# Optimization experiments

Hardware: AMD Instinct MI355X
Metric: run time of the kernel (lower is better)

The kernel has to match this reference:

```python
import jax, jax.numpy as jnp
import numpy as np

NUM_HEADS = 16
EMBED_DIM = 1024
LN_EPS = 1e-5


def setup_inputs() -> dict:
    key = jax.random.key(0)
    ks = jax.random.split(key, 9)
    B, S, D = 4, 1024, EMBED_DIM
    return {
        "query": jax.random.normal(ks[0], (B, S, D), dtype=jnp.float32),
        "key": jax.random.normal(ks[1], (B, S, D), dtype=jnp.float32),
        "value": jax.random.normal(ks[2], (B, S, D), dtype=jnp.float32),
        "W_query": 0.01 * jax.random.normal(ks[3], (D, D), dtype=jnp.float32),
        "W_key": 0.01 * jax.random.normal(ks[4], (D, D), dtype=jnp.float32),
        "W_value": 0.01 * jax.random.normal(ks[5], (D, D), dtype=jnp.float32),
        "W_output": 0.01 * jax.random.normal(ks[6], (D, D), dtype=jnp.float32),
        "ln_gamma": jnp.ones((D,), dtype=jnp.float32),
        "ln_beta": jnp.zeros((D,), dtype=jnp.float32),
        "mask": 1,
    }


def _split_heads(x):
    # [B,S,D] -> [H,B,S,d]; torch split(dim=-1)+stack(dim=0) gives head h = cols h*d:(h+1)*d
    B, S, D = x.shape
    d = D // NUM_HEADS
    return jnp.moveaxis(x.reshape(B, S, NUM_HEADS, d), 2, 0)


def reference(query, key, value, W_query, W_key, W_value, W_output, ln_gamma, ln_beta, mask):
    B, S, D = query.shape
    d = D // NUM_HEADS
    q = _split_heads(query @ W_query)   # [H,B,S,d]
    k = _split_heads(key @ W_key)       # [H,B,S,d]
    v = _split_heads(value @ W_value)   # [H,B,S,d]
    scale = jnp.asarray(np.sqrt(d), dtype=q.dtype)
    scores = jnp.einsum("hbqd,hbkd->hbqk", q, k) / scale  # [H,B,S,S]
    attn = jax.nn.softmax(scores, axis=-1)
    if mask:
        # post-hoc causal: zero strict upper triangle, then renormalize rows
        tri = jnp.tril(jnp.ones((S, S), dtype=bool))
        attn = jnp.where(tri, attn, 0.0)
        attn = attn / jnp.sum(attn, axis=-1, keepdims=True)
    ws = jnp.einsum("hbqk,hbkd->hbqd", attn, v)            # [H,B,S,d]
    concat = jnp.moveaxis(ws, 0, 2).reshape(B, S, D)       # [B,S,D]
    out = concat @ W_output + query                        # residual
    mu = jnp.mean(out, axis=-1, keepdims=True)
    var = jnp.var(out, axis=-1, keepdims=True)
    out = (out - mu) / jnp.sqrt(var + LN_EPS) * ln_gamma + ln_beta
    return out, attn
```

## Files before the change

kernel.cpp:

```cpp
#include <hip/hip_runtime.h>
#include <hip/hip_bf16.h>

#define Bn   4
#define Sn   1024
#define Dn   1024
#define Hn   16
#define dHn  64
#define HB   (Hn * Bn)
#define MROWS (Bn * Sn)

typedef __attribute__((ext_vector_type(8))) short bf16x8;
typedef __attribute__((ext_vector_type(4))) float f32x4;

__device__ __forceinline__ ushort f2bf(float x) {
  union { float f; unsigned u; } v; v.f = x;
  unsigned r = v.u + 0x7FFF + ((v.u >> 16) & 1);
  return (ushort)(r >> 16);
}
__device__ __forceinline__ float bf2f(ushort u) {
  union { unsigned u; float f; } v; v.u = ((unsigned)u) << 16; return v.f;
}

__device__ __forceinline__ void load_lds16(const void* g, void* l) {
  __builtin_amdgcn_global_load_lds(
      (const __attribute__((address_space(1))) unsigned int*)g,
      (__attribute__((address_space(3))) unsigned int*)l, 16, 0, 0);
}

__global__ __launch_bounds__(256) void cast_kernel(
    const float* __restrict__ in, ushort* __restrict__ out) {
  int idx = blockIdx.x * 256 + threadIdx.x;
  float4 v = *(const float4*)&in[(size_t)idx * 4];
  ushort4 o;
  o.x = f2bf(v.x); o.y = f2bf(v.y); o.z = f2bf(v.z); o.w = f2bf(v.w);
  *(ushort4*)&out[(size_t)idx * 4] = o;
}

__global__ __launch_bounds__(256) void transpose_cast_kernel(
    const float* __restrict__ W, ushort* __restrict__ WT, int K, int N) {
  __shared__ ushort T[64 * 72];
  const int k0 = blockIdx.y * 64, n0 = blockIdx.x * 64;
  const int t = threadIdx.x;
  const int r = t >> 4, c4 = (t & 15) * 4;
#pragma unroll
  for (int i = 0; i < 4; ++i) {
    int row = r + i * 16;
    float4 v = *(const float4*)&W[(size_t)(k0 + row) * N + n0 + c4];
    T[(c4 + 0) * 72 + row] = f2bf(v.x);
    T[(c4 + 1) * 72 + row] = f2bf(v.y);
    T[(c4 + 2) * 72 + row] = f2bf(v.z);
    T[(c4 + 3) * 72 + row] = f2bf(v.w);
  }
  __syncthreads();
#pragma unroll
  for (int i = 0; i < 2; ++i) {
    int c = t + i * 256;
    int n = c >> 3, kg = (c & 7) * 8;
    *(ulonglong2*)&WT[(size_t)(n0 + n) * K + k0 + kg] =
        *(const ulonglong2*)&T[n * 72 + kg];
  }
}

template <int MODE>
__global__ __launch_bounds__(256) void gemm_bt(
    const ushort* __restrict__ A, const ushort* __restrict__ Bt,
    const float* __restrict__ resid, void* __restrict__ Cout,
    int M, int N, int K) {
  __shared__ ushort lds[MODE == 1 ? 17408 : 8192];
  ushort* As = lds;
  ushort* Bs = lds + 4096;
  const int t = threadIdx.x;
  const int w = t >> 6, lane = t & 63;
  const int wr = (w >> 1) * 64, wc = (w & 1) * 64;
  const int l16 = lane & 15, quad = lane >> 4;
  const int m0 = blockIdx.y * 128, n0 = blockIdx.x * 128;
  const int srow = (lane >> 2);
  const int scol = (lane & 3) * 8;
  f32x4 acc[4][4] = {};
  for (int k0 = 0; k0 < K; k0 += 32) {
#pragma unroll
    for (int c = 0; c < 2; ++c) {
      int row = w * 32 + c * 16 + srow;
      load_lds16(&A[(size_t)(m0 + row) * K + k0 + scol],
                 &As[(size_t)w * 1024 + c * 512]);
      load_lds16(&Bt[(size_t)(n0 + row) * K + k0 + scol],
                 &Bs[(size_t)w * 1024 + c * 512]);
    }
    __syncthreads();
    bf16x8 af[4], bfr[4];
#pragma unroll
    for (int mi = 0; mi < 4; ++mi)
      af[mi] = *(const bf16x8*)&As[(wr + mi * 16 + l16) * 32 + quad * 8];
#pragma unroll
    for (int ni = 0; ni < 4; ++ni)
      bfr[ni] = *(const bf16x8*)&Bs[(wc + ni * 16 + l16) * 32 + quad * 8];
#pragma unroll
    for (int mi = 0; mi < 4; ++mi)
#pragma unroll
      for (int ni = 0; ni < 4; ++ni)
        acc[mi][ni] = __builtin_amdgcn_mfma_f32_16x16x32_bf16(
            af[mi], bfr[ni], acc[mi][ni], 0, 0, 0);
    __syncthreads();
  }
  if (MODE == 0) {
    float* C = (float*)Cout;
#pragma unroll
    for (int mi = 0; mi < 4; ++mi)
#pragma unroll
      for (int ni = 0; ni < 4; ++ni) {
        int n = n0 + wc + ni * 16 + l16;
#pragma unroll
        for (int r = 0; r < 4; ++r) {
          int m = m0 + wr + mi * 16 + quad * 4 + r;
          float v = acc[mi][ni][r];
          if (resid) v += resid[(size_t)m * N + n];
          C[(size_t)m * N + n] = v;
        }
      }
  } else if (MODE == 2) {
    ushort* C = (ushort*)Cout;
#pragma unroll
    for (int mi = 0; mi < 4; ++mi) {
      int mb = m0 + wr + mi * 16 + quad * 4;
      int b = mb >> 10, s = mb & 1023;
#pragma unroll
      for (int ni = 0; ni < 4; ++ni) {
        int n = n0 + wc + ni * 16 + l16;
        ushort4 o;
        o.x = f2bf(acc[mi][ni][0]);
        o.y = f2bf(acc[mi][ni][1]);
        o.z = f2bf(acc[mi][ni][2]);
        o.w = f2bf(acc[mi][ni][3]);
        *(ushort4*)&C[((size_t)b * N + n) * Sn + s] = o;
      }
    }
  } else {
    ushort* Cs = lds;
#pragma unroll
    for (int mi = 0; mi < 4; ++mi)
#pragma unroll
      for (int ni = 0; ni < 4; ++ni) {
        int col = wc + ni * 16 + l16;
#pragma unroll
        for (int r = 0; r < 4; ++r)
          Cs[(wr + mi * 16 + quad * 4 + r) * 136 + col] = f2bf(acc[mi][ni][r]);
      }
    __syncthreads();
    ushort* C = (ushort*)Cout;
#pragma unroll
    for (int i = 0; i < 8; ++i) {
      int c = t + i * 256;
      int row = c >> 4, cg = (c & 15) * 8;
      *(ulonglong2*)&C[(size_t)(m0 + row) * N + n0 + cg] =
          *(const ulonglong2*)&Cs[row * 136 + cg];
    }
  }
}

__global__ __launch_bounds__(256, 2) void attn_fused(
    const ushort* __restrict__ Qp, const ushort* __restrict__ Kp,
    const ushort* __restrict__ Vt, float* __restrict__ attn,
    ushort* __restrict__ Cc) {
  const int hb = blockIdx.x, qt = blockIdx.y;
  const int h = hb >> 2, b = hb & 3;
  const int q0 = qt * 64;
  const int nkt = (qt >> 1) + 1;

  __shared__ ushort Qs[64 * 72];
  __shared__ ushort Ks[128 * 72];
  __shared__ ushort Vs[64 * 136];
  __shared__ ushort Ps[64 * 136];

  const int t = threadIdx.x;
  const int w = t >> 6, lane = t & 63;
  const int l16 = lane & 15, quad = lane >> 4;

  for (int ktz = nkt; ktz < 8; ++ktz) {
    const int k0 = ktz * 128;
#pragma unroll
    for (int i = 0; i < 4; ++i) {
      int cc = t + i * 256;
      int row = cc >> 4, cg = (cc & 15) * 8;
      float* dst = &attn[((size_t)hb * Sn + q0 + row) * Sn + k0 + cg];
      *(float4*)&dst[0] = make_float4(0.f, 0.f, 0.f, 0.f);
      *(float4*)&dst[4] = make_float4(0.f, 0.f, 0.f, 0.f);
    }
  }

#pragma unroll
  for (int i = 0; i < 2; ++i) {
    int cc = t + i * 256;
    int row = cc >> 3, cg = (cc & 7) * 8;
    *(ulonglong2*)&Qs[row * 72 + cg] =
        *(const ulonglong2*)&Qp[((size_t)b * Sn + q0 + row) * Dn + h * dHn + cg];
  }

  float m_run[4], l_run[4];
#pragma unroll
  for (int r = 0; r < 4; ++r) { m_run[r] = -3e38f; l_run[r] = 0.f; }

  for (int kt = 0; kt < nkt; ++kt) {
    const int k0 = kt * 128;
#pragma unroll
    for (int i = 0; i < 4; ++i) {
      int cc = t + i * 256;
      int row = cc >> 3, cg = (cc & 7) * 8;
      *(ulonglong2*)&Ks[row * 72 + cg] =
          *(const ulonglong2*)&Kp[((size_t)b * Sn + k0 + row) * Dn + h * dHn + cg];
    }
    __syncthreads();
    bf16x8 aq[2];
#pragma unroll
    for (int ks = 0; ks < 2; ++ks)
      aq[ks] = *(const bf16x8*)&Qs[(w * 16 + l16) * 72 + ks * 32 + quad * 8];
    f32x4 s[8];
#pragma unroll
    for (int ni = 0; ni < 8; ++ni) {
      f32x4 a = {};
#pragma unroll
      for (int ks = 0; ks < 2; ++ks) {
        bf16x8 bk = *(const bf16x8*)&Ks[(ni * 16 + l16) * 72 + ks * 32 + quad * 8];
        a = __builtin_amdgcn_mfma_f32_16x16x32_bf16(aq[ks], bk, a, 0, 0, 0);
      }
      s[ni] = a;
    }
    float tmax[4] = {-3e38f, -3e38f, -3e38f, -3e38f};
#pragma unroll
    for (int ni = 0; ni < 8; ++ni)
#pragma unroll
      for (int r = 0; r < 4; ++r) {
        int kg = k0 + ni * 16 + l16;
        int qg = q0 + w * 16 + quad * 4 + r;
        float v = (kg <= qg) ? s[ni][r] * 0.125f : -3e38f;
        s[ni][r] = v;
        tmax[r] = fmaxf(tmax[r], v);
      }
#pragma unroll
    for (int d = 1; d < 16; d <<= 1)
#pragma unroll
      for (int r = 0; r < 4; ++r)
        tmax[r] = fmaxf(tmax[r], __shfl_xor(tmax[r], d));
    float mnew[4], tsum[4] = {0.f, 0.f, 0.f, 0.f};
#pragma unroll
    for (int r = 0; r < 4; ++r) mnew[r] = fmaxf(m_run[r], tmax[r]);
#pragma unroll
    for (int ni = 0; ni < 8; ++ni)
#pragma unroll
      for (int r = 0; r < 4; ++r) tsum[r] += __expf(s[ni][r] - mnew[r]);
#pragma unroll
    for (int d = 1; d < 16; d <<= 1)
#pragma unroll
      for (int r = 0; r < 4; ++r) tsum[r] += __shfl_xor(tsum[r], d);
#pragma unroll
    for (int r = 0; r < 4; ++r) {
      l_run[r] = l_run[r] * __expf(m_run[r] - mnew[r]) + tsum[r];
      m_run[r] = mnew[r];
    }
    __syncthreads();
  }
  float inv_l[4];
#pragma unroll
  for (int r = 0; r < 4; ++r) inv_l[r] = 1.0f / l_run[r];

  f32x4 acc_o[4] = {};
  for (int kt = 0; kt < nkt; ++kt) {
    const int k0 = kt * 128;
#pragma unroll
    for (int i = 0; i < 4; ++i) {
      int cc = t + i * 256;
      int row = cc >> 3, cg = (cc & 7) * 8;
      *(ulonglong2*)&Ks[row * 72 + cg] =
          *(const ulonglong2*)&Kp[((size_t)b * Sn + k0 + row) * Dn + h * dHn + cg];
    }
#pragma unroll
    for (int i = 0; i < 4; ++i) {
      int cc = t + i * 256;
      int row = cc >> 4, cg = (cc & 15) * 8;
      *(ulonglong2*)&Vs[row * 136 + cg] =
          *(const ulonglong2*)&Vt[((size_t)b * Dn + h * dHn + row) * Sn + k0 + cg];
    }
    __syncthreads();
    bf16x8 aq[2];
#pragma unroll
    for (int ks = 0; ks < 2; ++ks)
      aq[ks] = *(const bf16x8*)&Qs[(w * 16 + l16) * 72 + ks * 32 + quad * 8];
    f32x4 s[8];
#pragma unroll
    for (int ni = 0; ni < 8; ++ni) {
      f32x4 a = {};
#pragma unroll
      for (int ks = 0; ks < 2; ++ks) {
        bf16x8 bk = *(const bf16x8*)&Ks[(ni * 16 + l16) * 72 + ks * 32 + quad * 8];
        a = __builtin_amdgcn_mfma_f32_16x16x32_bf16(aq[ks], bk, a, 0, 0, 0);
      }
      s[ni] = a;
    }
#pragma unroll
    for (int ni = 0; ni < 8; ++ni)
#pragma unroll
      for (int r = 0; r < 4; ++r) {
        int kg = k0 + ni * 16 + l16;
        int qg = q0 + w * 16 + quad * 4 + r;
        float v = (kg <= qg) ? s[ni][r] * 0.125f : -3e38f;
        float p = __expf(v - m_run[r]) * inv_l[r];
        Ps[(w * 16 + quad * 4 + r) * 136 + ni * 16 + l16] = f2bf(p);
      }
#pragma unroll
    for (int ks = 0; ks < 4; ++ks) {
      bf16x8 ap = *(const bf16x8*)&Ps[(w * 16 + l16) * 136 + ks * 32 + quad * 8];
#pragma unroll
      for (int ni = 0; ni < 4; ++ni) {
        bf16x8 bv = *(const bf16x8*)&Vs[(ni * 16 + l16) * 136 + ks * 32 + quad * 8];
        acc_o[ni] = __builtin_amdgcn_mfma_f32_16x16x32_bf16(ap, bv, acc_o[ni], 0, 0, 0);
      }
    }
    __syncthreads();
#pragma unroll
    for (int i = 0; i < 4; ++i) {
      int cc = t + i * 256;
      int row = cc >> 4, cg = (cc & 15) * 8;
      bf16x8 pv = *(const bf16x8*)&Ps[row * 136 + cg];
      float* dst = &attn[((size_t)hb * Sn + q0 + row) * Sn + k0 + cg];
      *(float4*)&dst[0] = make_float4(bf2f((ushort)pv[0]), bf2f((ushort)pv[1]),
                                      bf2f((ushort)pv[2]), bf2f((ushort)pv[3]));
      *(float4*)&dst[4] = make_float4(bf2f((ushort)pv[4]), bf2f((ushort)pv[5]),
                                      bf2f((ushort)pv[6]), bf2f((ushort)pv[7]));
    }
  }
#pragma unroll
  for (int ni = 0; ni < 4; ++ni)
#pragma unroll
    for (int r = 0; r < 4; ++r) {
      int q = q0 + w * 16 + quad * 4 + r;
      int j = ni * 16 + l16;
      Cc[((size_t)b * Sn + q) * Dn + h * dHn + j] = f2bf(acc_o[ni][r]);
    }
}

__global__ __launch_bounds__(256) void ln_kernel(
    float* __restrict__ out, const float* __restrict__ gamma,
    const float* __restrict__ beta) {
  const int row = blockIdx.x;
  float* p = out + (size_t)row * Dn;
  const int t = threadIdx.x;
  float v[4];
  float s = 0.f, s2 = 0.f;
#pragma unroll
  for (int i = 0; i < 4; ++i) {
    v[i] = p[t + i * 256];
    s += v[i];
    s2 += v[i] * v[i];
  }
  __shared__ float r1[256], r2[256];
  r1[t] = s; r2[t] = s2;
  __syncthreads();
  for (int st = 128; st > 0; st >>= 1) {
    if (t < st) { r1[t] += r1[t + st]; r2[t] += r2[t + st]; }
    __syncthreads();
  }
  const float mu  = r1[0] * (1.0f / Dn);
  const float var = r2[0] * (1.0f / Dn) - mu * mu;
  const float rstd = rsqrtf(var + 1e-5f);
#pragma unroll
  for (int i = 0; i < 4; ++i) {
    int c = t + i * 256;
    p[c] = (v[i] - mu) * rstd * gamma[c] + beta[c];
  }
}

extern "C" void kernel_launch(void* const* d_in, const int* in_sizes, int n_in,
                              void* d_out, int out_size, void* d_ws, size_t ws_size,
                              hipStream_t stream) {
  const float* q_in  = (const float*)d_in[0];
  const float* k_in  = (const float*)d_in[1];
  const float* v_in  = (const float*)d_in[2];
  const float* Wq    = (const float*)d_in[3];
  const float* Wk    = (const float*)d_in[4];
  const float* Wv    = (const float*)d_in[5];
  const float* Wo    = (const float*)d_in[6];
  const float* gamma = (const float*)d_in[7];
  const float* beta  = (const float*)d_in[8];

  float* out  = (float*)d_out;
  float* attn = out + (size_t)Bn * Sn * Dn;

  const size_t QN = (size_t)Bn * Sn * Dn;
  ushort* ws  = (ushort*)d_ws;
  ushort* qbf = ws;
  ushort* kbf = qbf + QN;
  ushort* vbf = kbf + QN;
  ushort* WqT = vbf + QN;
  ushort* WkT = WqT + (size_t)Dn * Dn;
  ushort* WvT = WkT + (size_t)Dn * Dn;
  ushort* WoT = WvT + (size_t)Dn * Dn;
  ushort* Qp  = WoT + (size_t)Dn * Dn;
  ushort* Kp  = Qp + QN;
  ushort* Vt  = Kp + QN;
  ushort* Cc  = Vt + QN;

  cast_kernel<<<QN / 1024, 256, 0, stream>>>(q_in, qbf);
  cast_kernel<<<QN / 1024, 256, 0, stream>>>(k_in, kbf);
  cast_kernel<<<QN / 1024, 256, 0, stream>>>(v_in, vbf);

  dim3 tg(Dn / 64, Dn / 64);
  transpose_cast_kernel<<<tg, 256, 0, stream>>>(Wq, WqT, Dn, Dn);
  transpose_cast_kernel<<<tg, 256, 0, stream>>>(Wk, WkT, Dn, Dn);
  transpose_cast_kernel<<<tg, 256, 0, stream>>>(Wv, WvT, Dn, Dn);
  transpose_cast_kernel<<<tg, 256, 0, stream>>>(Wo, WoT, Dn, Dn);

  dim3 gg(Dn / 128, MROWS / 128);
  gemm_bt<1><<<gg, 256, 0, stream>>>(qbf, WqT, nullptr, Qp, MROWS, Dn, Dn);
  gemm_bt<1><<<gg, 256, 0, stream>>>(kbf, WkT, nullptr, Kp, MROWS, Dn, Dn);
  gemm_bt<2><<<gg, 256, 0, stream>>>(vbf, WvT, nullptr, Vt, MROWS, Dn, Dn);

  attn_fused<<<dim3(HB, Sn / 64), 256, 0, stream>>>(Qp, Kp, Vt, attn, Cc);

  gemm_bt<0><<<gg, 256, 0, stream>>>(Cc, WoT, q_in, out, MROWS, Dn, Dn);
  ln_kernel<<<MROWS, 256, 0, stream>>>(out, gamma, beta);
}
```

Measured before the change: 538.1 us.

## Batch cast, transpose and QKV GEMM launches; hold Q fragments in registers

Merges the three input cast launches, the four weight transpose launches and the three QKV projection GEMMs into single launches that pick their operand by grid z/y index. This cuts launch count and lets the QKV GEMMs fill the GPU together. In the attention kernel, Q fragments are now loaded once from global memory straight into registers instead of staged through LDS. That shrinks LDS use so occupancy can go from 2 to 3 blocks per CU, at the cost of more register pressure. The output GEMM is split into its own specialized kernel.

```diff
diff --git a/kernel.cpp b/kernel.cpp
--- a/kernel.cpp
+++ b/kernel.cpp
@@ -8,6 +8,7 @@
 #define dHn  64
 #define HB   (Hn * Bn)
 #define MROWS (Bn * Sn)
+#define QNE  ((size_t)Bn * Sn * Dn)
 
 typedef __attribute__((ext_vector_type(8))) short bf16x8;
 typedef __attribute__((ext_vector_type(4))) float f32x4;
@@ -27,17 +28,25 @@
       (__attribute__((address_space(3))) unsigned int*)l, 16, 0, 0);
 }
 
-__global__ __launch_bounds__(256) void cast_kernel(
-    const float* __restrict__ in, ushort* __restrict__ out) {
+__global__ __launch_bounds__(256) void cast3_kernel(
+    const float* __restrict__ q, const float* __restrict__ k,
+    const float* __restrict__ v, ushort* __restrict__ outb) {
+  const float* in = blockIdx.y == 0 ? q : (blockIdx.y == 1 ? k : v);
+  ushort* out = outb + (size_t)blockIdx.y * QNE;
   int idx = blockIdx.x * 256 + threadIdx.x;
-  float4 v = *(const float4*)&in[(size_t)idx * 4];
+  float4 x = *(const float4*)&in[(size_t)idx * 4];
   ushort4 o;
-  o.x = f2bf(v.x); o.y = f2bf(v.y); o.z = f2bf(v.z); o.w = f2bf(v.w);
+  o.x = f2bf(x.x); o.y = f2bf(x.y); o.z = f2bf(x.z); o.w = f2bf(x.w);
   *(ushort4*)&out[(size_t)idx * 4] = o;
 }
 
-__global__ __launch_bounds__(256) void transpose_cast_kernel(
-    const float* __restrict__ W, ushort* __restrict__ WT, int K, int N) {
+__global__ __launch_bounds__(256) void transpose4_kernel(
+    const float* __restrict__ Wq, const float* __restrict__ Wk,
+    const float* __restrict__ Wv, const float* __restrict__ Wo,
+    ushort* __restrict__ WTb) {
+  const int z = blockIdx.z;
+  const float* W = z == 0 ? Wq : (z == 1 ? Wk : (z == 2 ? Wv : Wo));
+  ushort* WT = WTb + (size_t)z * Dn * Dn;
   __shared__ ushort T[64 * 72];
   const int k0 = blockIdx.y * 64, n0 = blockIdx.x * 64;
   const int t = threadIdx.x;
@@ -45,7 +54,7 @@
 #pragma unroll
   for (int i = 0; i < 4; ++i) {
     int row = r + i * 16;
-    float4 v = *(const float4*)&W[(size_t)(k0 + row) * N + n0 + c4];
+    float4 v = *(const float4*)&W[(size_t)(k0 + row) * Dn + n0 + c4];
     T[(c4 + 0) * 72 + row] = f2bf(v.x);
     T[(c4 + 1) * 72 + row] = f2bf(v.y);
     T[(c4 + 2) * 72 + row] = f2bf(v.z);
@@ -56,17 +65,21 @@
   for (int i = 0; i < 2; ++i) {
     int c = t + i * 256;
     int n = c >> 3, kg = (c & 7) * 8;
-    *(ulonglong2*)&WT[(size_t)(n0 + n) * K + k0 + kg] =
+    *(ulonglong2*)&WT[(size_t)(n0 + n) * Dn + k0 + kg] =
         *(const ulonglong2*)&T[n * 72 + kg];
   }
 }
 
-template <int MODE>
-__global__ __launch_bounds__(256) void gemm_bt(
-    const ushort* __restrict__ A, const ushort* __restrict__ Bt,
-    const float* __restrict__ resid, void* __restrict__ Cout,
-    int M, int N, int K) {
-  __shared__ ushort lds[MODE == 1 ? 17408 : 8192];
+__global__ __launch_bounds__(256, 3) void qkv_gemm(
+    const ushort* __restrict__ Ab, const ushort* __restrict__ Bb,
+    ushort* __restrict__ Cb) {
+  const int z = blockIdx.z;
+  const ushort* A  = Ab + (size_t)z * QNE;
+  const ushort* Bt = Bb + (size_t)z * Dn * Dn;
+  ushort* C        = Cb + (size_t)z * QNE;
+  const int M = MROWS, N = Dn, K = Dn;
+
+  __shared__ ushort lds[17408];
   ushort* As = lds;
   ushort* Bs = lds + 4096;
   const int t = threadIdx.x;
@@ -102,23 +115,7 @@
             af[mi], bfr[ni], acc[mi][ni], 0, 0, 0);
     __syncthreads();
   }
-  if (MODE == 0) {
-    float* C = (float*)Cout;
-#pragma unroll
-    for (int mi = 0; mi < 4; ++mi)
-#pragma unroll
-      for (int ni = 0; ni < 4; ++ni) {
-        int n = n0 + wc + ni * 16 + l16;
-#pragma unroll
-        for (int r = 0; r < 4; ++r) {
-          int m = m0 + wr + mi * 16 + quad * 4 + r;
-          float v = acc[mi][ni][r];
-          if (resid) v += resid[(size_t)m * N + n];
-          C[(size_t)m * N + n] = v;
-        }
-      }
-  } else if (MODE == 2) {
-    ushort* C = (ushort*)Cout;
+  if (z == 2) {
 #pragma unroll
     for (int mi = 0; mi < 4; ++mi) {
       int mb = m0 + wr + mi * 16 + quad * 4;
@@ -146,7 +143,6 @@
           Cs[(wr + mi * 16 + quad * 4 + r) * 136 + col] = f2bf(acc[mi][ni][r]);
       }
     __syncthreads();
-    ushort* C = (ushort*)Cout;
 #pragma unroll
     for (int i = 0; i < 8; ++i) {
       int c = t + i * 256;
@@ -157,7 +153,62 @@
   }
 }
 
-__global__ __launch_bounds__(256, 2) void attn_fused(
+__global__ __launch_bounds__(256) void gemm_out(
+    const ushort* __restrict__ A, const ushort* __restrict__ Bt,
+    const float* __restrict__ resid, float* __restrict__ C,
+    int M, int N, int K) {
+  __shared__ ushort lds[8192];
+  ushort* As = lds;
+  ushort* Bs = lds + 4096;
+  const int t = threadIdx.x;
+  const int w = t >> 6, lane = t & 63;
+  const int wr = (w >> 1) * 64, wc = (w & 1) * 64;
+  const int l16 = lane & 15, quad = lane >> 4;
+  const int m0 = blockIdx.y * 128, n0 = blockIdx.x * 128;
+  const int srow = (lane >> 2);
+  const int scol = (lane & 3) * 8;
+  f32x4 acc[4][4] = {};
+  for (int k0 = 0; k0 < K; k0 += 32) {
+#pragma unroll
+    for (int c = 0; c < 2; ++c) {
+      int row = w * 32 + c * 16 + srow;
+      load_lds16(&A[(size_t)(m0 + row) * K + k0 + scol],
+                 &As[(size_t)w * 1024 + c * 512]);
+      load_lds16(&Bt[(size_t)(n0 + row) * K + k0 + scol],
+                 &Bs[(size_t)w * 1024 + c * 512]);
+    }
+    __syncthreads();
+    bf16x8 af[4], bfr[4];
+#pragma unroll
+    for (int mi = 0; mi < 4; ++mi)
+      af[mi] = *(const bf16x8*)&As[(wr + mi * 16 + l16) * 32 + quad * 8];
+#pragma unroll
+    for (int ni = 0; ni < 4; ++ni)
+      bfr[ni] = *(const bf16x8*)&Bs[(wc + ni * 16 + l16) * 32 + quad * 8];
+#pragma unroll
+    for (int mi = 0; mi < 4; ++mi)
+#pragma unroll
+      for (int ni = 0; ni < 4; ++ni)
+        acc[mi][ni] = __builtin_amdgcn_mfma_f32_16x16x32_bf16(
+            af[mi], bfr[ni], acc[mi][ni], 0, 0, 0);
+    __syncthreads();
+  }
+#pragma unroll
+  for (int mi = 0; mi < 4; ++mi)
+#pragma unroll
+    for (int ni = 0; ni < 4; ++ni) {
+      int n = n0 + wc + ni * 16 + l16;
+#pragma unroll
+      for (int r = 0; r < 4; ++r) {
+        int m = m0 + wr + mi * 16 + quad * 4 + r;
+        float v = acc[mi][ni][r];
+        v += resid[(size_t)m * N + n];
+        C[(size_t)m * N + n] = v;
+      }
+    }
+}
+
+__global__ __launch_bounds__(256, 3) void attn_fused(
     const ushort* __restrict__ Qp, const ushort* __restrict__ Kp,
     const ushort* __restrict__ Vt, float* __restrict__ attn,
     ushort* __restrict__ Cc) {
@@ -166,7 +217,6 @@
   const int q0 = qt * 64;
   const int nkt = (qt >> 1) + 1;
 
-  __shared__ ushort Qs[64 * 72];
   __shared__ ushort Ks[128 * 72];
   __shared__ ushort Vs[64 * 136];
   __shared__ ushort Ps[64 * 136];
@@ -187,13 +237,11 @@
     }
   }
 
-#pragma unroll
-  for (int i = 0; i < 2; ++i) {
-    int cc = t + i * 256;
-    int row = cc >> 3, cg = (cc & 7) * 8;
-    *(ulonglong2*)&Qs[row * 72 + cg] =
-        *(const ulonglong2*)&Qp[((size_t)b * Sn + q0 + row) * Dn + h * dHn + cg];
-  }
+  bf16x8 aq[2];
+#pragma unroll
+  for (int ks = 0; ks < 2; ++ks)
+    aq[ks] = *(const bf16x8*)&Qp[((size_t)b * Sn + q0 + w * 16 + l16) * Dn +
+                                 h * dHn + ks * 32 + quad * 8];
 
   float m_run[4], l_run[4];
 #pragma unroll
@@ -209,10 +257,6 @@
           *(const ulonglong2*)&Kp[((size_t)b * Sn + k0 + row) * Dn + h * dHn + cg];
     }
     __syncthreads();
-    bf16x8 aq[2];
-#pragma unroll
-    for (int ks = 0; ks < 2; ++ks)
-      aq[ks] = *(const bf16x8*)&Qs[(w * 16 + l16) * 72 + ks * 32 + quad * 8];
     f32x4 s[8];
 #pragma unroll
     for (int ni = 0; ni < 8; ++ni) {
@@ -280,10 +324,6 @@
           *(const ulonglong2*)&Vt[((size_t)b * Dn + h * dHn + row) * Sn + k0 + cg];
     }
     __syncthreads();
-    bf16x8 aq[2];
-#pragma unroll
-    for (int ks = 0; ks < 2; ++ks)
-      aq[ks] = *(const bf16x8*)&Qs[(w * 16 + l16) * 72 + ks * 32 + quad * 8];
     f32x4 s[8];
 #pragma unroll
     for (int ni = 0; ni < 8; ++ni) {
@@ -384,37 +424,28 @@
   float* out  = (float*)d_out;
   float* attn = out + (size_t)Bn * Sn * Dn;
 
-  const size_t QN = (size_t)Bn * Sn * Dn;
   ushort* ws  = (ushort*)d_ws;
   ushort* qbf = ws;
-  ushort* kbf = qbf + QN;
-  ushort* vbf = kbf + QN;
-  ushort* WqT = vbf + QN;
+  ushort* kbf = qbf + QNE;
+  ushort* vbf = kbf + QNE;
+  ushort* WqT = vbf + QNE;
   ushort* WkT = WqT + (size_t)Dn * Dn;
   ushort* WvT = WkT + (size_t)Dn * Dn;
   ushort* WoT = WvT + (size_t)Dn * Dn;
   ushort* Qp  = WoT + (size_t)Dn * Dn;
-  ushort* Kp  = Qp + QN;
-  ushort* Vt  = Kp + QN;
-  ushort* Cc  = Vt + QN;
-
-  cast_kernel<<<QN / 1024, 256, 0, stream>>>(q_in, qbf);
-  cast_kernel<<<QN / 1024, 256, 0, stream>>>(k_in, kbf);
-  cast_kernel<<<QN / 1024, 256, 0, stream>>>(v_in, vbf);
-
-  dim3 tg(Dn / 64, Dn / 64);
-  transpose_cast_kernel<<<tg, 256, 0, stream>>>(Wq, WqT, Dn, Dn);
-  transpose_cast_kernel<<<tg, 256, 0, stream>>>(Wk, WkT, Dn, Dn);
-  transpose_cast_kernel<<<tg, 256, 0, stream>>>(Wv, WvT, Dn, Dn);
-  transpose_cast_kernel<<<tg, 256, 0, stream>>>(Wo, WoT, Dn, Dn);
-
-  dim3 gg(Dn / 128, MROWS / 128);
-  gemm_bt<1><<<gg, 256, 0, stream>>>(qbf, WqT, nullptr, Qp, MROWS, Dn, Dn);
-  gemm_bt<1><<<gg, 256, 0, stream>>>(kbf, WkT, nullptr, Kp, MROWS, Dn, Dn);
-  gemm_bt<2><<<gg, 256, 0, stream>>>(vbf, WvT, nullptr, Vt, MROWS, Dn, Dn);
+  ushort* Kp  = Qp + QNE;
+  ushort* Vt  = Kp + QNE;
+  ushort* Cc  = Vt + QNE;
+
+  (void)kbf; (void)vbf; (void)WkT; (void)WvT; (void)Kp;
+
+  cast3_kernel<<<dim3(QNE / 1024, 3), 256, 0, stream>>>(q_in, k_in, v_in, qbf);
+  transpose4_kernel<<<dim3(Dn / 64, Dn / 64, 4), 256, 0, stream>>>(Wq, Wk, Wv, Wo, WqT);
+
+  qkv_gemm<<<dim3(Dn / 128, MROWS / 128, 3), 256, 0, stream>>>(qbf, WqT, Qp);
 
   attn_fused<<<dim3(HB, Sn / 64), 256, 0, stream>>>(Qp, Kp, Vt, attn, Cc);
 
-  gemm_bt<0><<<gg, 256, 0, stream>>>(Cc, WoT, q_in, out, MROWS, Dn, Dn);
+  gemm_out<<<dim3(Dn / 128, MROWS / 128), 256, 0, stream>>>(Cc, WoT, q_in, out, MROWS, Dn, Dn);
   ln_kernel<<<MROWS, 256, 0, stream>>>(out, gamma, beta);
 }
```

After: 464.4 us. 1.16x faster.
